# Performance work log

Measured on AMD Instinct MI355X. Metric: run time of the kernel, lower is better.

## Reference

```python
import jax, jax.numpy as jnp
import numpy as np
import math

B, T, D = 4, 2048, 1024
H, DK, DV = 4, 128, 256
KD, VD = H * DK, H * DV
LOG_T_REF = math.log(512.0)
EPS = 1e-5


def setup_inputs() -> dict:
    key = jax.random.key(0)
    ks = jax.random.split(key, 8)
    hs = jax.random.normal(ks[0], (B, T, D), dtype=jnp.float32)
    Wq = jax.random.normal(ks[1], (KD, D), dtype=jnp.float32) / math.sqrt(D)
    Wk = jax.random.normal(ks[2], (KD, D), dtype=jnp.float32) / math.sqrt(D)
    Wv = jax.random.normal(ks[3], (VD, D), dtype=jnp.float32) / math.sqrt(D)
    Wg = jax.random.normal(ks[4], (VD, D), dtype=jnp.float32) / math.sqrt(D)
    Wa = jax.random.normal(ks[5], (KD, D), dtype=jnp.float32) / math.sqrt(D)
    Wo = jax.random.normal(ks[6], (D, VD), dtype=jnp.float32) / math.sqrt(VD)
    # _post_init: A_log_base = 0, A_log_delta = log(exp(gap)-1+1e-6), gap = log(16)/(H-1)
    gap = math.log(16.0) / (H - 1)
    A_log_base = jnp.zeros((), dtype=jnp.float32)
    A_log_delta = jnp.full((H - 1,), math.log(math.exp(gap) - 1.0 + 1e-6), dtype=jnp.float32)
    # dt_bias init (inverse-softplus of dt sampled loguniform in [1e-3, 1e-1])
    rng = np.random.default_rng(0)
    dt = np.exp(rng.random(KD) * (math.log(0.1) - math.log(0.001)) + math.log(0.001))
    dt = np.clip(dt, 1e-4, None)
    dt_bias = jnp.asarray(dt + np.log(-np.expm1(-dt)), dtype=jnp.float32)
    g_norm_weight = jnp.ones((VD,), dtype=jnp.float32)
    return {"hidden_states": hs, "Wq": Wq, "Wk": Wk, "Wv": Wv, "Wg": Wg, "Wa": Wa,
            "Wo": Wo, "A_log_base": A_log_base, "A_log_delta": A_log_delta,
            "dt_bias": dt_bias, "g_norm_weight": g_norm_weight}


def _gla_forward(hidden_states, Wq, Wk, Wv, Wg, Wa, Wo, A_log_base, A_log_delta, dt_bias, g_norm_weight):
    b, t, _ = hidden_states.shape
    q = (hidden_states @ Wq.T).reshape(b, t, H, DK)
    k = (hidden_states @ Wk.T).reshape(b, t, H, DK)
    v = (hidden_states @ Wv.T).reshape(b, t, H, DV)
    a = (hidden_states @ Wa.T).reshape(b, t, H, DK)

    # geometric spectral allocation: A_log[h] = base + cumsum(softplus(delta))
    A_log = A_log_base + jnp.concatenate([jnp.zeros((1,), dtype=A_log_delta.dtype),
                                          jnp.cumsum(jax.nn.softplus(A_log_delta))])
    # per-head log-decay gate: gk = -exp(A_log) * softplus(a + dt_bias)  [b,t,h,dk]
    gk = -jnp.exp(A_log)[None, None, :, None] * jax.nn.softplus(a + dt_bias.reshape(H, DK)[None, None])

    # analytical position-adaptive alpha
    cum = A_log - A_log[0]
    kk = jnp.arange(H, dtype=A_log.dtype)
    mean_gap = cum[-1] / (H - 1)
    taper = (H - 1 - kk) / (H - 1)
    alpha = jnp.clip(taper + (cum - kk * mean_gap) / LOG_T_REF, 0.0, 1.0)  # [H]
    pos = jnp.arange(1, t + 1, dtype=jnp.float32)
    gk = gk * (pos[:, None] ** (-alpha[None, :]))[None, :, :, None]

    # gated linear attention recurrence: S_t = exp(gk_t)*S_{t-1} + k_t^T v_t ; o_t = q_t S_t
    scale = DK ** -0.5
    qT = jnp.moveaxis(q, 1, 0) * scale  # [t,b,h,dk]
    kT = jnp.moveaxis(k, 1, 0)
    vT = jnp.moveaxis(v, 1, 0)
    gT = jnp.moveaxis(gk, 1, 0)

    def step(S, inp):
        qt, kt, vt, gt = inp
        S = S * jnp.exp(gt)[..., None] + kt[..., None] * vt[..., None, :]  # [b,h,dk,dv]
        ot = jnp.einsum('bhk,bhkv->bhv', qt, S)
        return S, ot

    S0 = jnp.zeros((b, H, DK, DV), dtype=jnp.float32)
    _, oT = jax.lax.scan(step, S0, (qT, kT, vT, gT))
    o = jnp.moveaxis(oT, 0, 1)  # [b,t,h,dv]

    # fused RMSNorm + swish output gate (per head over dv)
    g = (hidden_states @ Wg.T).reshape(b, t, H, DV)
    o = o * jax.lax.rsqrt(jnp.mean(o * o, axis=-1, keepdims=True) + EPS)
    o = o * g_norm_weight.reshape(H, DV)[None, None] * (g * jax.nn.sigmoid(g))
    return o.reshape(b, t, VD) @ Wo.T


def reference(hidden_states, Wq, Wk, Wv, Wg, Wa, Wo, A_log_base, A_log_delta, dt_bias, g_norm_weight):
    return _gla_forward(hidden_states, Wq, Wk, Wv, Wg, Wa, Wo, A_log_base, A_log_delta, dt_bias, g_norm_weight)
```

## Files before the change

kernel.cpp:

```cpp
#include <hip/hip_runtime.h>
#include <math.h>

#define Bn   4
#define Tn   2048
#define Dn   1024
#define Hn   4
#define DKn  128
#define DVn  256
#define KDn  512
#define VDn  1024
#define NROWS 8192
#define NCC  32
#define CLEN 64
#define LOG_T_REF_F 6.2383246250395075f

using bf16x8 = __attribute__((ext_vector_type(8))) short;
using f32x4  = __attribute__((ext_vector_type(4))) float;

__device__ __forceinline__ float softplus_f(float x) {
    return fmaxf(x, 0.0f) + log1pf(expf(-fabsf(x)));
}
__device__ __forceinline__ ushort f2bf(float f) {
    unsigned u = __float_as_uint(f);
    u = (u + 0x7fffu + ((u >> 16) & 1u)) >> 16;
    return (ushort)u;
}
__device__ __forceinline__ float bf2f(ushort u) {
    return __uint_as_float((unsigned)u << 16);
}
__device__ __forceinline__ void gload16(const void* g, void* l) {
    __builtin_amdgcn_global_load_lds(
        (const __attribute__((address_space(1))) unsigned*)g,
        (__attribute__((address_space(3))) unsigned*)l, 16, 0, 0);
}

struct CastArgs {
    const float* src[7];
    ushort* dst[7];
    int cum[8];
};
__global__ __launch_bounds__(256) void cast_all(CastArgs a) {
    const int total = a.cum[7];
    for (int i = blockIdx.x * 256 + threadIdx.x; i < total; i += gridDim.x * 256) {
        int s = 0;
        #pragma unroll
        for (int k = 1; k < 7; ++k) s += (i >= a.cum[k]) ? 1 : 0;
        const int off = i - a.cum[s];
        float4 v = *(const float4*)&a.src[s][(size_t)off * 4];
        ushort4 u;
        u.x = f2bf(v.x); u.y = f2bf(v.y); u.z = f2bf(v.z); u.w = f2bf(v.w);
        *(ushort4*)&a.dst[s][(size_t)off * 4] = u;
    }
}

template<int NX>
__global__ __launch_bounds__(512) void mm_big(const ushort* __restrict__ A,
    const ushort* __restrict__ Bw, float* __restrict__ C,
    float* __restrict__ Cv, ushort* __restrict__ C2, float* __restrict__ Eo,
    const float* __restrict__ dt_bias, const float* __restrict__ A_log_base,
    const float* __restrict__ A_log_delta)
{
    extern __shared__ __align__(16) char smem2[];
    ushort* sm = (ushort*)smem2;
    const int raw = blockIdx.x;
    const int nwg = NX * 32;
    const int l = (raw & 7) * (nwg >> 3) + (raw >> 3);
    const int bx = l % NX, by = l / NX;
    const int tid = threadIdx.x;
    const int w = tid >> 6, lane = tid & 63;
    const int l15 = lane & 15, lg = lane >> 4;
    const int wr = w >> 2, wc = w & 3;
    const int row0 = by << 8, col0 = bx << 8;

    const ushort* Asrc = A  + (size_t)(row0 + lane) * Dn + w * 8;
    const ushort* Bsrc = Bw + (size_t)(col0 + lane) * Dn + w * 8;

    f32x4 acc[8][4];
    #pragma unroll
    for (int m = 0; m < 8; ++m)
        #pragma unroll
        for (int n = 0; n < 4; ++n)
            acc[m][n] = (f32x4){0.f, 0.f, 0.f, 0.f};

    #define STAGE(buf, kt)                                                        \
    {                                                                             \
        ushort* ab_ = sm + (buf) * 32768 + w * 2048;                              \
        ushort* bb_ = ab_ + 16384;                                                \
        _Pragma("unroll")                                                         \
        for (int g_ = 0; g_ < 4; ++g_) {                                          \
            gload16(Asrc + (size_t)g_ * 64 * Dn + (kt), ab_ + g_ * 512);          \
            gload16(Bsrc + (size_t)g_ * 64 * Dn + (kt), bb_ + g_ * 512);          \
        }                                                                         \
    }

    STAGE(0, 0)
    for (int it = 0; it < 16; ++it) {
        const int cur = it & 1;
        if (it < 15) {
            STAGE(cur ^ 1, (it + 1) * 64)
            asm volatile("s_waitcnt vmcnt(8)" ::: "memory");
        } else {
            asm volatile("s_waitcnt vmcnt(0)" ::: "memory");
        }
        asm volatile("s_barrier" ::: "memory");
        const ushort* ab = sm + cur * 32768;
        const ushort* bb = ab + 16384;
        #pragma unroll
        for (int ks = 0; ks < 2; ++ks) {
            bf16x8 af[8], bv[4];
            #pragma unroll
            for (int m = 0; m < 8; ++m)
                af[m] = *(const bf16x8*)(ab + (ks * 4 + lg) * 2048
                                            + (wr * 128 + m * 16 + l15) * 8);
            #pragma unroll
            for (int n = 0; n < 4; ++n)
                bv[n] = *(const bf16x8*)(bb + (ks * 4 + lg) * 2048
                                            + (wc * 64 + n * 16 + l15) * 8);
            #pragma unroll
            for (int m = 0; m < 8; ++m)
                #pragma unroll
                for (int n = 0; n < 4; ++n)
                    acc[m][n] = __builtin_amdgcn_mfma_f32_16x16x32_bf16(af[m], bv[n], acc[m][n], 0, 0, 0);
        }
        asm volatile("s_barrier" ::: "memory");
    }
    #undef STAGE

    if (col0 >= 1024 && col0 < 1536) {
        const float base_ = A_log_base[0];
        const float s0 = softplus_f(A_log_delta[0]);
        const float s1 = softplus_f(A_log_delta[1]);
        const float s2 = softplus_f(A_log_delta[2]);
        const float c3 = s0 + s1 + s2;
        const float mg = c3 * (1.0f / 3.0f);
        #pragma unroll
        for (int m = 0; m < 8; ++m) {
            const int row = row0 + wr * 128 + m * 16 + lg * 4;
            float pf[4];
            #pragma unroll
            for (int r = 0; r < 4; ++r) {
                const int t = (row + r) & (Tn - 1);
                pf[r] = logf((float)(t + 1));
            }
            #pragma unroll
            for (int n = 0; n < 4; ++n) {
                const int dk = col0 - 1024 + wc * 64 + n * 16 + l15;
                const int h = dk >> 7;
                const float cumh = (h == 0) ? 0.f : (h == 1) ? s0 : (h == 2) ? s0 + s1 : c3;
                float alpha = (float)(3 - h) * (1.0f / 3.0f)
                            + (cumh - (float)h * mg) * (1.0f / LOG_T_REF_F);
                alpha = fminf(fmaxf(alpha, 0.0f), 1.0f);
                const float expA = expf(base_ + cumh);
                const float db = dt_bias[dk];
                #pragma unroll
                for (int r = 0; r < 4; ++r) {
                    const float p = expf(-alpha * pf[r]);
                    Eo[(size_t)(row + r) * KDn + dk] =
                        -expA * softplus_f(acc[m][n][r] + db) * p;
                }
            }
        }
    } else if (col0 >= 2560) {
        #pragma unroll
        for (int m = 0; m < 8; ++m) {
            const int row = row0 + wr * 128 + m * 16 + lg * 4;
            #pragma unroll
            for (int n = 0; n < 4; ++n) {
                const int col = col0 - 2560 + wc * 64 + n * 16 + l15;
                #pragma unroll
                for (int r = 0; r < 4; ++r)
                    C2[(size_t)(row + r) * 1024 + col] = f2bf(acc[m][n][r]);
            }
        }
    } else if (col0 >= 1536) {
        #pragma unroll
        for (int m = 0; m < 8; ++m) {
            const int row = row0 + wr * 128 + m * 16 + lg * 4;
            #pragma unroll
            for (int n = 0; n < 4; ++n) {
                const int col = col0 - 1536 + wc * 64 + n * 16 + l15;
                #pragma unroll
                for (int r = 0; r < 4; ++r)
                    Cv[(size_t)(row + r) * 1024 + col] = acc[m][n][r];
            }
        }
    } else {
        const float s = (col0 < 512) ? 0.08838834764831845f : 1.0f;
        #pragma unroll
        for (int m = 0; m < 8; ++m) {
            const int row = row0 + wr * 128 + m * 16 + lg * 4;
            #pragma unroll
            for (int n = 0; n < 4; ++n) {
                const int col = col0 + wc * 64 + n * 16 + l15;
                #pragma unroll
                for (int r = 0; r < 4; ++r)
                    C[(size_t)(row + r) * 1024 + col] = acc[m][n][r] * s;
            }
        }
    }
}

__global__ __launch_bounds__(256) void mm_out(const ushort* __restrict__ A,
    const ushort* __restrict__ Bw, float* __restrict__ C)
{
    __shared__ __align__(16) ushort As[8][128][8];
    __shared__ __align__(16) ushort Bs[8][128][8];
    const int raw = blockIdx.x;
    const int l = (raw & 7) * 64 + (raw >> 3);
    const int bx = l % 8, by = l / 8;
    const int tid = threadIdx.x;
    const int lane = tid & 63, w = tid >> 6;
    const int l15 = lane & 15, lg = lane >> 4;
    const int wr = (w >> 1) << 6, wc = (w & 1) << 6;
    const int row0 = by << 7, col0 = bx << 7;

    const ushort* A0 = A  + (size_t)(row0 + lane) * Dn + w * 8;
    const ushort* A1 = A  + (size_t)(row0 + 64 + lane) * Dn + w * 8;
    const ushort* B0 = Bw + (size_t)(col0 + lane) * Dn + w * 8;
    const ushort* B1 = Bw + (size_t)(col0 + 64 + lane) * Dn + w * 8;

    f32x4 acc[4][4];
    #pragma unroll
    for (int m = 0; m < 4; ++m)
        #pragma unroll
        for (int n = 0; n < 4; ++n)
            acc[m][n] = (f32x4){0.f, 0.f, 0.f, 0.f};

    for (int kt = 0; kt < Dn; kt += 64) {
        __syncthreads();
        gload16(A0 + kt,      &As[w][0][0]);
        gload16(A0 + kt + 32, &As[w + 4][0][0]);
        gload16(A1 + kt,      &As[w][64][0]);
        gload16(A1 + kt + 32, &As[w + 4][64][0]);
        gload16(B0 + kt,      &Bs[w][0][0]);
        gload16(B0 + kt + 32, &Bs[w + 4][0][0]);
        gload16(B1 + kt,      &Bs[w][64][0]);
        gload16(B1 + kt + 32, &Bs[w + 4][64][0]);
        __syncthreads();
        #pragma unroll
        for (int ks = 0; ks < 2; ++ks) {
            bf16x8 af[4], bv[4];
            #pragma unroll
            for (int m = 0; m < 4; ++m)
                af[m] = *(const bf16x8*)&As[ks * 4 + lg][wr + m * 16 + l15][0];
            #pragma unroll
            for (int n = 0; n < 4; ++n)
                bv[n] = *(const bf16x8*)&Bs[ks * 4 + lg][wc + n * 16 + l15][0];
            #pragma unroll
            for (int m = 0; m < 4; ++m)
                #pragma unroll
                for (int n = 0; n < 4; ++n)
                    acc[m][n] = __builtin_amdgcn_mfma_f32_16x16x32_bf16(af[m], bv[n], acc[m][n], 0, 0, 0);
        }
    }
    #pragma unroll
    for (int m = 0; m < 4; ++m) {
        const int row = row0 + wr + m * 16 + lg * 4;
        #pragma unroll
        for (int n = 0; n < 4; ++n) {
            const int col = col0 + wc + n * 16 + l15;
            #pragma unroll
            for (int r = 0; r < 4; ++r)
                C[(size_t)(row + r) * 1024 + col] = acc[m][n][r];
        }
    }
}

__global__ __launch_bounds__(1024) void gla_chunk(
    float* qk, const float* __restrict__ Gb, const float* __restrict__ vb,
    float* __restrict__ o, float* __restrict__ Sl, float* __restrict__ Dc)
{
    extern __shared__ __align__(16) char smem[];
    float*  g    = (float*)smem;
    ushort* qraw = (ushort*)(smem + 33792);
    ushort* kraw = (ushort*)(smem + 51200);
    ushort* Qb   = (ushort*)(smem + 68608);
    ushort* Koff = (ushort*)(smem + 86016);
    ushort* KhT  = (ushort*)(smem + 112128);
    ushort* At   = (ushort*)(smem + 130560);
    ushort* VT   = (ushort*)smem;
    float*  qsum = (float*)(smem + 86016);

    const int bid = blockIdx.x;
    const int co = bid >> 4, bh = bid & 15;
    const int b = bh >> 2, h = bh & 3;
    const int tid = threadIdx.x;
    const int w = tid >> 6, lane = tid & 63;
    const int l15 = lane & 15, lg = lane >> 4;
    const size_t rowbase = (size_t)(b * Tn + co * CLEN);

    float c16[16];
    int dk1 = 0, qr1 = 0;
    if (tid < 512) {
        dk1 = tid & 127; qr1 = tid >> 7;
        const float* gp = Gb + (rowbase + qr1 * 16) * 512 + h * 128 + dk1;
        float run = 0.f;
        #pragma unroll
        for (int s = 0; s < 16; ++s) { run += gp[(size_t)s * 512]; c16[s] = run; }
        qsum[qr1 * 128 + dk1] = run;
    }
    __syncthreads();
    if (tid < 512) {
        float pre = 0.f;
        for (int r = 0; r < qr1; ++r) pre += qsum[r * 128 + dk1];
        #pragma unroll
        for (int s = 0; s < 16; ++s) g[(qr1 * 16 + s) * 132 + dk1] = c16[s] + pre;
    }
    __syncthreads();

    #pragma unroll
    for (int it = 0; it < 8; ++it) {
        const int idx = tid + it * 1024;
        const int t = idx >> 7, dk = idx & 127;
        const float gi = g[t * 132 + dk];
        const size_t qaddr = (rowbase + t) * 1024 + h * 128 + dk;
        const float qv = qk[qaddr];
        const float gr = (t < 16) ? 0.f : g[(16 * (t >> 4) - 1) * 132 + dk];
        Qb[t * 136 + dk] = f2bf(qv * __expf(gi - gr));
        qraw[t * 136 + dk] = f2bf(qv);
        qk[qaddr] = qv * __expf(gi);
        const float kv = qk[qaddr + 512];
        kraw[t * 136 + dk] = f2bf(kv);
        KhT[dk * 72 + t] = f2bf(kv * __expf(g[63 * 132 + dk] - gi));
        if (t < 16) Koff[t * 136 + dk]        = f2bf(kv * __expf(g[15 * 132 + dk] - gi));
        if (t < 32) Koff[(16 + t) * 136 + dk] = f2bf(kv * __expf(g[31 * 132 + dk] - gi));
        if (t < 48) Koff[(48 + t) * 136 + dk] = f2bf(kv * __expf(g[47 * 132 + dk] - gi));
    }
    for (int i = tid; i < 2304; i += 1024) ((int*)At)[i] = 0;
    if (tid < 128)
        Dc[(co * 16 + bh) * 128 + tid] = __expf(g[63 * 132 + tid]);
    __syncthreads();

    if (w < 6) {
        const int Tt[6] = {16, 32, 32, 48, 48, 48};
        const int Ss[6] = { 0,  0, 16,  0, 16, 32};
        const int Kb[6] = { 0, 16, 16, 48, 48, 48};
        const int T = Tt[w], S = Ss[w], KB = Kb[w];
        f32x4 acc = (f32x4){0.f, 0.f, 0.f, 0.f};
        #pragma unroll
        for (int kk = 0; kk < 4; ++kk) {
            bf16x8 a  = *(const bf16x8*)&Qb[(T + l15) * 136 + kk * 32 + lg * 8];
            bf16x8 bb = *(const bf16x8*)&Koff[(KB + S + l15) * 136 + kk * 32 + lg * 8];
            acc = __builtin_amdgcn_mfma_f32_16x16x32_bf16(a, bb, acc, 0, 0, 0);
        }
        #pragma unroll
        for (int r = 0; r < 4; ++r)
            At[(T + lg * 4 + r) * 72 + S + l15] = f2bf(acc[r]);
    } else if (w < 14) {
        const int d = (w - 6) >> 1, hf = (w - 6) & 1;
        #pragma unroll
        for (int pp = 0; pp < 2; ++pp) {
            const int p = hf * 128 + pp * 64 + lane;
            const int i_ = p >> 4, j_ = p & 15;
            if (j_ <= i_) {
                const int ti = d * 16 + i_, tj = d * 16 + j_;
                float a = 0.f;
                for (int dk = 0; dk < 128; ++dk) {
                    const float qf = bf2f(qraw[ti * 136 + dk]);
                    const float kf = bf2f(kraw[tj * 136 + dk]);
                    a += qf * kf * __expf(g[ti * 132 + dk] - g[tj * 132 + dk]);
                }
                At[ti * 72 + tj] = f2bf(a);
            }
        }
    }
    __syncthreads();

    {
        const int dv4 = (tid & 63) * 4, tseg = tid >> 6;
        float4 vv[4];
        #pragma unroll
        for (int s = 0; s < 4; ++s)
            vv[s] = *(const float4*)&vb[(rowbase + tseg * 4 + s) * 1024 + h * 256 + dv4];
        const float* vf = (const float*)vv;
        #pragma unroll
        for (int c = 0; c < 4; ++c) {
            int lo = (unsigned)f2bf(vf[0 * 4 + c]) | ((unsigned)f2bf(vf[1 * 4 + c]) << 16);
            int hi = (unsigned)f2bf(vf[2 * 4 + c]) | ((unsigned)f2bf(vf[3 * 4 + c]) << 16);
            *(int2*)((char*)VT + (size_t)(dv4 + c) * 144 + tseg * 8) = make_int2(lo, hi);
        }
    }
    __syncthreads();

    float* sp = Sl + (((size_t)co * 16 + bh) << 15);
    for (int id = w; id < 192; id += 16) {
        if (id < 64) {
            const int mt = id >> 4, nt = id & 15;
            f32x4 acc = (f32x4){0.f, 0.f, 0.f, 0.f};
            #pragma unroll
            for (int kk = 0; kk < 2; ++kk) {
                bf16x8 a  = *(const bf16x8*)&At[(mt * 16 + l15) * 72 + kk * 32 + lg * 8];
                bf16x8 bb = *(const bf16x8*)&VT[(nt * 16 + l15) * 72 + kk * 32 + lg * 8];
                acc = __builtin_amdgcn_mfma_f32_16x16x32_bf16(a, bb, acc, 0, 0, 0);
            }
            #pragma unroll
            for (int r = 0; r < 4; ++r)
                o[(rowbase + mt * 16 + lg * 4 + r) * 1024 + h * 256 + nt * 16 + l15] = acc[r];
        } else {
            const int sid = id - 64;
            const int mt = sid >> 4, nt = sid & 15;
            f32x4 acc = (f32x4){0.f, 0.f, 0.f, 0.f};
            #pragma unroll
            for (int kk = 0; kk < 2; ++kk) {
                bf16x8 a  = *(const bf16x8*)&KhT[(mt * 16 + l15) * 72 + kk * 32 + lg * 8];
                bf16x8 bb = *(const bf16x8*)&VT[(nt * 16 + l15) * 72 + kk * 32 + lg * 8];
                acc = __builtin_amdgcn_mfma_f32_16x16x32_bf16(a, bb, acc, 0, 0, 0);
            }
            #pragma unroll
            for (int r = 0; r < 4; ++r)
                sp[(size_t)(mt * 16 + lg * 4 + r) * 256 + nt * 16 + l15] = acc[r];
        }
    }
}

__global__ __launch_bounds__(256) void combine(float* __restrict__ Sl,
                                               const float* __restrict__ Dc) {
    const int bh = blockIdx.y;
    const int e4 = blockIdx.x * 256 + threadIdx.x;
    const int dk = e4 >> 6;
    float4 s = make_float4(0.f, 0.f, 0.f, 0.f);
    #pragma unroll 4
    for (int c = 0; c < NCC; ++c) {
        float4* p = (float4*)(Sl + (((size_t)c * 16 + bh) << 15)) + e4;
        float4 local = *p;
        const float d = Dc[(c * 16 + bh) * DKn + dk];
        *p = s;
        s.x = s.x * d + local.x;  s.y = s.y * d + local.y;
        s.z = s.z * d + local.z;  s.w = s.w * d + local.w;
    }
}

__global__ __launch_bounds__(256, 4) void fixup(const float* __restrict__ qt,
    const float* __restrict__ Sl, float* __restrict__ o)
{
    __shared__ __align__(16) float Aq[16][68];
    __shared__ __align__(16) float Bs[16][68];
    const int raw = blockIdx.x;
    const int l = (raw & 7) * 256 + (raw >> 3);
    const int dvt = l & 3, bh = (l >> 2) & 15, co = l >> 6;
    const int b = bh >> 2, h = bh & 3;
    const int tid = threadIdx.x;
    const int tx = tid & 15, ty = tid >> 4;
    const int t0 = co * CLEN;
    const int dv0 = dvt * 64;

    const float* qbase = qt + (size_t)(b * Tn + t0) * 1024 + h * 128;
    const float* sbase = Sl + (((size_t)co * 16 + bh) << 15) + dv0;

    float acc[4][4] = {};
    for (int k0 = 0; k0 < DKn; k0 += 16) {
        __syncthreads();
        {
            const int t = tid >> 2, kk4 = (tid & 3) << 2;
            float4 a = *(const float4*)&qbase[(size_t)t * 1024 + k0 + kk4];
            Aq[kk4 + 0][t] = a.x; Aq[kk4 + 1][t] = a.y;
            Aq[kk4 + 2][t] = a.z; Aq[kk4 + 3][t] = a.w;
        }
        {
            const int dk = tid >> 4, dvq = (tid & 15) << 2;
            *(float4*)&Bs[dk][dvq] = *(const float4*)&sbase[(size_t)(k0 + dk) * 256 + dvq];
        }
        __syncthreads();
        #pragma unroll
        for (int kk = 0; kk < 16; ++kk) {
            float4 a  = *(const float4*)&Aq[kk][ty * 4];
            float4 bv = *(const float4*)&Bs[kk][tx * 4];
            float ar[4] = {a.x, a.y, a.z, a.w};
            float br[4] = {bv.x, bv.y, bv.z, bv.w};
            #pragma unroll
            for (int i = 0; i < 4; ++i)
                #pragma unroll
                for (int j = 0; j < 4; ++j)
                    acc[i][j] += ar[i] * br[j];
        }
    }
    float* obp = o + (size_t)(b * Tn + t0) * 1024 + h * 256 + dv0;
    #pragma unroll
    for (int i = 0; i < 4; ++i) {
        float* row = obp + (size_t)(ty * 4 + i) * 1024 + tx * 4;
        float4 c = *(float4*)row;
        c.x += acc[i][0]; c.y += acc[i][1];
        c.z += acc[i][2]; c.w += acc[i][3];
        *(float4*)row = c;
    }
}

__global__ __launch_bounds__(256) void rms_gate(const float* __restrict__ o,
    const ushort* __restrict__ gbf, const float* __restrict__ wt,
    ushort* __restrict__ obf)
{
    const int tid = threadIdx.x;
    const int w = tid >> 6, lane = tid & 63;
    const int row = blockIdx.x * 4 + w;
    const int n = row >> 2, h = row & 3;
    const size_t ob_base = (size_t)n * VDn + h * DVn + lane * 4;

    float4 o4 = *(const float4*)&o[ob_base];
    float ss = o4.x*o4.x + o4.y*o4.y + o4.z*o4.z + o4.w*o4.w;
    #pragma unroll
    for (int m = 1; m < 64; m <<= 1) ss += __shfl_xor(ss, m);
    const float r = rsqrtf(ss * (1.0f / DVn) + 1e-5f);

    ushort4 gu = *(const ushort4*)&gbf[ob_base];
    float gx = bf2f(gu.x), gy = bf2f(gu.y), gz = bf2f(gu.z), gw = bf2f(gu.w);
    float4 w4 = *(const float4*)&wt[h * DVn + lane * 4];
    ushort4 u;
    u.x = f2bf(o4.x * r * w4.x * (gx / (1.0f + expf(-gx))));
    u.y = f2bf(o4.y * r * w4.y * (gy / (1.0f + expf(-gy))));
    u.z = f2bf(o4.z * r * w4.z * (gz / (1.0f + expf(-gz))));
    u.w = f2bf(o4.w * r * w4.w * (gw / (1.0f + expf(-gw))));
    *(ushort4*)&obf[ob_base] = u;
}

extern "C" void kernel_launch(void* const* d_in, const int* in_sizes, int n_in,
                              void* d_out, int out_size, void* d_ws, size_t ws_size,
                              hipStream_t stream) {
    const float* hs          = (const float*)d_in[0];
    const float* Wq          = (const float*)d_in[1];
    const float* Wk          = (const float*)d_in[2];
    const float* Wv          = (const float*)d_in[3];
    const float* Wg          = (const float*)d_in[4];
    const float* Wa          = (const float*)d_in[5];
    const float* Wo          = (const float*)d_in[6];
    const float* A_log_base  = (const float*)d_in[7];
    const float* A_log_delta = (const float*)d_in[8];
    const float* dt_bias     = (const float*)d_in[9];
    const float* gnw         = (const float*)d_in[10];
    float* out = (float*)d_out;

    char* ws = (char*)d_ws;
    float*  qk   = (float*)(ws);
    float*  vb   = (float*)(ws + ((size_t)32  << 20));
    float*  Gbuf = (float*)(ws + ((size_t)64  << 20));
    float*  Sl   = (float*)(ws + ((size_t)80  << 20));
    float*  ob   = (float*)(ws + ((size_t)144 << 20));
    ushort* hsb  = (ushort*)(ws + ((size_t)144 << 20));
    ushort* gbf  = (ushort*)(ws + ((size_t)176 << 20));
    ushort* Wcat = (ushort*)(ws + ((size_t)192 << 20));
    ushort* Wob  = (ushort*)(ws + ((size_t)199 << 20));
    float*  Dc   = (float*)(ws + ((size_t)201 << 20));
    ushort* obf  = (ushort*)qk;

    CastArgs ca;
    ca.src[0] = hs; ca.src[1] = Wq; ca.src[2] = Wk; ca.src[3] = Wa;
    ca.src[4] = Wv; ca.src[5] = Wg; ca.src[6] = Wo;
    ca.dst[0] = hsb;
    ca.dst[1] = Wcat;
    ca.dst[2] = Wcat + (size_t)512 * 1024;
    ca.dst[3] = Wcat + (size_t)1024 * 1024;
    ca.dst[4] = Wcat + (size_t)1536 * 1024;
    ca.dst[5] = Wcat + (size_t)2560 * 1024;
    ca.dst[6] = Wob;
    const int n4s[7] = {NROWS * Dn / 4, KDn * Dn / 4, KDn * Dn / 4, KDn * Dn / 4,
                        VDn * Dn / 4, VDn * Dn / 4, VDn * Dn / 4};
    ca.cum[0] = 0;
    for (int i = 0; i < 7; ++i) ca.cum[i + 1] = ca.cum[i] + n4s[i];
    cast_all<<<2048, 256, 0, stream>>>(ca);

    (void)hipFuncSetAttribute((const void*)mm_big<14>,
                              hipFuncAttributeMaxDynamicSharedMemorySize, 131072);
    mm_big<14><<<448, 512, 131072, stream>>>(hsb, Wcat, qk, vb, gbf, Gbuf,
                                             dt_bias, A_log_base, A_log_delta);

    (void)hipFuncSetAttribute((const void*)gla_chunk,
                              hipFuncAttributeMaxDynamicSharedMemorySize, 139776);
    gla_chunk<<<512, 1024, 139776, stream>>>(qk, Gbuf, vb, ob, Sl, Dc);
    combine<<<dim3(32, 16), 256, 0, stream>>>(Sl, Dc);
    fixup<<<2048, 256, 0, stream>>>(qk, Sl, ob);

    rms_gate<<<NROWS * Hn / 4, 256, 0, stream>>>(ob, gbf, gnw, obf);
    mm_out<<<512, 256, 0, stream>>>(obf, Wob, out);
}
```

Baseline: 310.7 us.

## Restructure projection GEMM mainloop into 4-stage ring buffer with split-phase MFMA

Replaces the double-buffered 64-wide K pipeline in the big projection GEMM with a 4-slot ring of 32-wide K stages, keeping three stages in flight. Each iteration is split into two halves. Each half issues the LDS fragment reads, launches the next global loads for A or B, then runs a burst of MFMAs at raised wave priority behind sched barriers. The aim is to hide global load latency and interleave LDS reads with MFMA issue, dropping the trailing barrier per step. In exchange it doubles the number of barrier-synchronized steps and relies on correct vmcnt accounting and ring-slot reuse.

```diff
diff --git a/kernel.cpp b/kernel.cpp
--- a/kernel.cpp
+++ b/kernel.cpp
@@ -61,7 +61,8 @@
     const float* __restrict__ A_log_delta)
 {
     extern __shared__ __align__(16) char smem2[];
-    ushort* sm = (ushort*)smem2;
+    ushort* Ar = (ushort*)smem2;
+    ushort* Br = Ar + 4 * 8192;
     const int raw = blockIdx.x;
     const int nwg = NX * 32;
     const int l = (raw & 7) * (nwg >> 3) + (raw >> 3);
@@ -72,8 +73,19 @@
     const int wr = w >> 2, wc = w & 3;
     const int row0 = by << 8, col0 = bx << 8;
 
-    const ushort* Asrc = A  + (size_t)(row0 + lane) * Dn + w * 8;
-    const ushort* Bsrc = Bw + (size_t)(col0 + lane) * Dn + w * 8;
+    const int ksw = w >> 1;
+    const int rg0 = (w & 1) * 2;
+    const ushort* Asrc = A  + (size_t)(row0 + rg0 * 64 + lane) * Dn + ksw * 8;
+    const ushort* Bsrc = Bw + (size_t)(col0 + rg0 * 64 + lane) * Dn + ksw * 8;
+    ushort* Adst0 = Ar + (ksw * 256 + rg0 * 64) * 8;
+    ushort* Bdst0 = Br + (ksw * 256 + rg0 * 64) * 8;
+
+#define STAGE_A(S) { ushort* d_ = Adst0 + ((S) & 3) * 8192;                    \
+    const ushort* s_ = Asrc + (size_t)(S) * 32;                                \
+    gload16(s_, d_); gload16(s_ + (size_t)64 * Dn, d_ + 512); }
+#define STAGE_B(S) { ushort* d_ = Bdst0 + ((S) & 3) * 8192;                    \
+    const ushort* s_ = Bsrc + (size_t)(S) * 32;                                \
+    gload16(s_, d_); gload16(s_ + (size_t)64 * Dn, d_ + 512); }
 
     f32x4 acc[8][4];
     #pragma unroll
@@ -82,49 +94,50 @@
         for (int n = 0; n < 4; ++n)
             acc[m][n] = (f32x4){0.f, 0.f, 0.f, 0.f};
 
-    #define STAGE(buf, kt)                                                        \
-    {                                                                             \
-        ushort* ab_ = sm + (buf) * 32768 + w * 2048;                              \
-        ushort* bb_ = ab_ + 16384;                                                \
-        _Pragma("unroll")                                                         \
-        for (int g_ = 0; g_ < 4; ++g_) {                                          \
-            gload16(Asrc + (size_t)g_ * 64 * Dn + (kt), ab_ + g_ * 512);          \
-            gload16(Bsrc + (size_t)g_ * 64 * Dn + (kt), bb_ + g_ * 512);          \
-        }                                                                         \
-    }
-
-    STAGE(0, 0)
-    for (int it = 0; it < 16; ++it) {
-        const int cur = it & 1;
-        if (it < 15) {
-            STAGE(cur ^ 1, (it + 1) * 64)
-            asm volatile("s_waitcnt vmcnt(8)" ::: "memory");
-        } else {
-            asm volatile("s_waitcnt vmcnt(0)" ::: "memory");
-        }
-        asm volatile("s_barrier" ::: "memory");
-        const ushort* ab = sm + cur * 32768;
-        const ushort* bb = ab + 16384;
-        #pragma unroll
-        for (int ks = 0; ks < 2; ++ks) {
-            bf16x8 af[8], bv[4];
-            #pragma unroll
-            for (int m = 0; m < 8; ++m)
-                af[m] = *(const bf16x8*)(ab + (ks * 4 + lg) * 2048
-                                            + (wr * 128 + m * 16 + l15) * 8);
+    STAGE_A(0) STAGE_B(0) STAGE_A(1) STAGE_B(1) STAGE_A(2) STAGE_B(2)
+
+    for (int S = 0; S < 32; ++S) {
+        if ((S & 1) == 0) {
+            if (S < 30) { asm volatile("s_waitcnt vmcnt(4)" ::: "memory"); }
+            else        { asm volatile("s_waitcnt vmcnt(0)" ::: "memory"); }
+        }
+        __builtin_amdgcn_s_barrier();
+        const ushort* As_ = Ar + (S & 3) * 8192 + lg * 2048;
+        const ushort* Bs_ = Br + (S & 3) * 8192 + lg * 2048;
+        bf16x8 af[4], bv[4];
+        #pragma unroll
+        for (int j = 0; j < 4; ++j)
+            af[j] = *(const bf16x8*)(As_ + (wr * 128 + j * 16 + l15) * 8);
+        #pragma unroll
+        for (int n = 0; n < 4; ++n)
+            bv[n] = *(const bf16x8*)(Bs_ + (wc * 64 + n * 16 + l15) * 8);
+        if (S <= 28) { STAGE_A(S + 3) }
+        asm volatile("s_waitcnt lgkmcnt(0)" ::: "memory");
+        __builtin_amdgcn_sched_barrier(0);
+        __builtin_amdgcn_s_setprio(1);
+        #pragma unroll
+        for (int j = 0; j < 4; ++j)
             #pragma unroll
             for (int n = 0; n < 4; ++n)
-                bv[n] = *(const bf16x8*)(bb + (ks * 4 + lg) * 2048
-                                            + (wc * 64 + n * 16 + l15) * 8);
-            #pragma unroll
-            for (int m = 0; m < 8; ++m)
-                #pragma unroll
-                for (int n = 0; n < 4; ++n)
-                    acc[m][n] = __builtin_amdgcn_mfma_f32_16x16x32_bf16(af[m], bv[n], acc[m][n], 0, 0, 0);
-        }
-        asm volatile("s_barrier" ::: "memory");
-    }
-    #undef STAGE
+                acc[j][n] = __builtin_amdgcn_mfma_f32_16x16x32_bf16(af[j], bv[n], acc[j][n], 0, 0, 0);
+        __builtin_amdgcn_s_setprio(0);
+        bf16x8 ag[4];
+        #pragma unroll
+        for (int j = 0; j < 4; ++j)
+            ag[j] = *(const bf16x8*)(As_ + (wr * 128 + 64 + j * 16 + l15) * 8);
+        if (S <= 28) { STAGE_B(S + 3) }
+        asm volatile("s_waitcnt lgkmcnt(0)" ::: "memory");
+        __builtin_amdgcn_sched_barrier(0);
+        __builtin_amdgcn_s_setprio(1);
+        #pragma unroll
+        for (int j = 0; j < 4; ++j)
+            #pragma unroll
+            for (int n = 0; n < 4; ++n)
+                acc[4 + j][n] = __builtin_amdgcn_mfma_f32_16x16x32_bf16(ag[j], bv[n], acc[4 + j][n], 0, 0, 0);
+        __builtin_amdgcn_s_setprio(0);
+    }
+#undef STAGE_A
+#undef STAGE_B
 
     if (col0 >= 1024 && col0 < 1536) {
         const float base_ = A_log_base[0];
```

New measurement: 300.7 us. 3.2% less time.
